# Kernel optimization log

Measured on AMD Instinct MI355X. Metric: run time of the kernel, lower is better.

The kernel has to match this reference:

```python
import jax, jax.numpy as jnp
import numpy as np
import math

B, S, HID, H, DH = 4, 1024, 1024, 16, 64  # batch, seq, hidden, heads, head_dim


def _rotate_half(x):
    x1, x2 = jnp.split(x, 2, axis=-1)
    return jnp.concatenate([-x2, x1], axis=-1)


def _apply_rope(t, freqs):
    # t: [B,H,S,DH], freqs: [S,rot_dim]; here rot_dim == DH so no pass-through part
    rot = freqs.shape[-1]
    cos_ = jnp.cos(freqs)[None, None, :, :].astype(t.dtype)
    sin_ = jnp.sin(freqs)[None, None, :, :].astype(t.dtype)
    t_rot, t_pass = t[..., :rot], t[..., rot:]
    t_rot = t_rot * cos_ + _rotate_half(t_rot) * sin_
    return jnp.concatenate([t_rot, t_pass], axis=-1)


def setup_inputs() -> dict:
    key = jax.random.key(0)
    ks = jax.random.split(key, 8)
    hidden_states = jax.random.normal(ks[0], (B, S, HID), dtype=jnp.float32)
    # additive mask: valid prefix of random length per batch row, -1e9 on padding
    lengths = jax.random.randint(ks[1], (B,), 3 * S // 4, S + 1)
    pos = jnp.arange(S)
    attention_mask = jnp.where(pos[None, :] < lengths[:, None], 0.0, -1e9)
    attention_mask = attention_mask.astype(jnp.float32)[:, None, None, :]  # [B,1,1,S]
    # rotary frequencies: standard RoPE angles, duplicated halves -> [S, DH]
    inv_freq = 1.0 / (10000.0 ** (jnp.arange(0, DH // 2, dtype=jnp.float32) / (DH // 2)))
    ang = pos.astype(jnp.float32)[:, None] * inv_freq[None, :]
    freqs = jnp.concatenate([ang, ang], axis=-1)  # [S, DH]
    sc = 0.02
    Wq = jax.random.normal(ks[2], (HID, HID), dtype=jnp.float32) * sc
    Wk = jax.random.normal(ks[3], (HID, HID), dtype=jnp.float32) * sc
    Wv = jax.random.normal(ks[4], (HID, HID), dtype=jnp.float32) * sc
    bq = jnp.zeros((HID,), dtype=jnp.float32)
    bk = jnp.zeros((HID,), dtype=jnp.float32)
    bv = jnp.zeros((HID,), dtype=jnp.float32)
    return dict(hidden_states=hidden_states, attention_mask=attention_mask, freqs=freqs,
                Wq=Wq, bq=bq, Wk=Wk, bk=bk, Wv=Wv, bv=bv)


def reference(hidden_states, attention_mask, freqs, Wq, bq, Wk, bk, Wv, bv):
    b, s, _ = hidden_states.shape
    # QKV projections -> [B,H,S,DH]
    q = (hidden_states @ Wq + bq).reshape(b, s, H, DH).transpose(0, 2, 1, 3)
    k = (hidden_states @ Wk + bk).reshape(b, s, H, DH).transpose(0, 2, 1, 3)
    v = (hidden_states @ Wv + bv).reshape(b, s, H, DH).transpose(0, 2, 1, 3)
    # inline RoPE on q and k (same freqs for both, as (rotary_pos_emb,)*2)
    q = _apply_rope(q, freqs)
    k = _apply_rope(k, freqs)
    scores = jnp.einsum('bhqd,bhkd->bhqk', q, k) / math.sqrt(DH)
    scores = scores + attention_mask  # additive mask broadcast over [B,H,S,S]
    probs = jax.nn.softmax(scores, axis=-1)
    # no_prob_mask filtering: zero out masked key columns
    probs = jnp.where(attention_mask < -1e-5, 0.0, probs)
    # dropout prob is 0.0 (eval) -> identity
    ctx = jnp.einsum('bhqk,bhkd->bhqd', probs, v)
    ctx = ctx.transpose(0, 2, 1, 3).reshape(b, s, H * DH)
    return ctx
```

## Files before the change

### kernel.cpp

```cpp
#include <hip/hip_runtime.h>
#include <hip/hip_bf16.h>
#include <cmath>

#define NB   4
#define NS   1024
#define NHID 1024
#define NH   16
#define NDH  64
#define QKV_PLANE (NB * NH * NS * NDH)

typedef __attribute__((ext_vector_type(8))) short bf16x8;
typedef __attribute__((ext_vector_type(4))) float f32x4;
typedef __attribute__((ext_vector_type(8))) unsigned short u16x8;

typedef __attribute__((address_space(1))) const void gv_t;
typedef __attribute__((address_space(3))) void       lv_t;

__device__ __forceinline__ void gload16(const void* g, void* l) {
    __builtin_amdgcn_global_load_lds((gv_t*)g, (lv_t*)l, 16, 0, 0);
}

__device__ __forceinline__ unsigned short f2b(float f) {
    union { float f; unsigned int u; } v; v.f = f;
    unsigned int r = (v.u + 0x7fff + ((v.u >> 16) & 1)) >> 16;
    return (unsigned short)r;
}

__device__ __forceinline__ unsigned int f2b2(float a, float b) {
    __hip_bfloat162 h = __float22bfloat162_rn(make_float2(a, b));
    union { __hip_bfloat162 h; unsigned int u; } v; v.h = h;
    return v.u;
}

__device__ __forceinline__ float fexp2(float x) {
#if __has_builtin(__builtin_amdgcn_exp2f)
    return __builtin_amdgcn_exp2f(x);
#else
    return exp2f(x);
#endif
}

__global__ __launch_bounds__(256) void prep_kernel(
    const float* __restrict__ hs, const float* __restrict__ freqs,
    const float* __restrict__ Wq, const float* __restrict__ Wk,
    const float* __restrict__ Wv,
    unsigned short* __restrict__ hsb, unsigned short* __restrict__ wt,
    float2* __restrict__ cs)
{
    const int z   = blockIdx.z;
    const int tid = threadIdx.x;

    if (z == 3) {
        const int bx = blockIdx.y * 16 + blockIdx.x;
        #pragma unroll
        for (int c = 0; c < 16; ++c) {
            const int idx = bx * 16384 + (c * 256 + tid) * 4;
            float4 v = *(const float4*)&hs[idx];
            ushort4 o;
            o.x = f2b(v.x); o.y = f2b(v.y); o.z = f2b(v.z); o.w = f2b(v.w);
            *(ushort4*)&hsb[idx] = o;
        }
        return;
    }
    if (z == 4) {
        const int bx = blockIdx.y * 16 + blockIdx.x;
        if (bx < 128) {
            const int id = bx * 256 + tid;
            const int s = id >> 5, d = id & 31;
            const float ang = freqs[s * NDH + d];
            float sn, cn;
            sincosf(ang, &sn, &cn);
            cs[id] = make_float2(cn, sn);
        }
        return;
    }

    const float* __restrict__ W = (z == 0) ? Wq : (z == 1) ? Wk : Wv;
    __shared__ float t[64][65];
    const int k0 = blockIdx.x * 64, n0 = blockIdx.y * 64;
    #pragma unroll
    for (int c = 0; c < 16; ++c) {
        const int flat = c * 256 + tid;
        const int r = flat >> 6, cc = flat & 63;
        t[r][cc] = W[(size_t)(k0 + r) * NHID + n0 + cc];
    }
    __syncthreads();
    #pragma unroll
    for (int c = 0; c < 16; ++c) {
        const int flat = c * 256 + tid;
        const int r = flat >> 6, cc = flat & 63;
        wt[(size_t)(z * 1024 + n0 + r) * NHID + k0 + cc] = f2b(t[cc][r]);
    }
}

__global__ __launch_bounds__(256) void fused_gemm_kernel(
    const unsigned short* __restrict__ hsb,
    const unsigned short* __restrict__ wt,
    const float2* __restrict__ cs,
    const float* __restrict__ bq, const float* __restrict__ bk,
    const float* __restrict__ bv,
    unsigned short* __restrict__ qkv)
{
    __shared__ short SH[16896];
    short* As = SH;
    short* Bs = SH + 8192;

    const int tid  = threadIdx.x;
    const int lane = tid & 63;
    const int wv   = __builtin_amdgcn_readfirstlane(tid >> 6);

    const int hw  = blockIdx.x + 24 * blockIdx.y;
    const int xcd = hw & 7;
    const int j   = hw >> 3;
    const int tx  = (xcd & 1) * 12 + (j % 12);
    const int ty  = (xcd >> 1) * 8 + (j / 12);

    const bool vmode = (tx >= 16);

    const unsigned short* Amat;
    const unsigned short* Bmat;
    int a_base, b_base, m0, n0, vb_ = 0;
    if (!vmode) {
        n0 = tx * 128;
        m0 = ty * 128;
        Amat = hsb;  a_base = m0;
        Bmat = wt;   b_base = n0;
    } else {
        m0  = (tx - 16) * 128;
        vb_ = ty >> 3;
        n0  = (ty & 7) * 128;
        Amat = wt;   a_base = 2048 + m0;
        Bmat = hsb;  b_base = vb_ * 1024 + n0;
    }

    const int ri  = lane >> 3;
    const int kcs = ((lane & 7) ^ ri) * 8;
    const unsigned short* gA[4];
    const unsigned short* gB[4];
    short* lA[4];
    short* lB[4];
    #pragma unroll
    for (int jj = 0; jj < 4; ++jj) {
        const int L = 4 * wv + jj;
        gA[jj] = Amat + (size_t)(a_base + L * 8 + ri) * NHID + kcs;
        gB[jj] = Bmat + (size_t)(b_base + L * 8 + ri) * NHID + kcs;
        lA[jj] = As + L * 512;
        lB[jj] = Bs + L * 512;
    }

    const int R  = (wv & 1) * 64;
    const int CW = (wv >> 1) * 64;
    const int c0 = lane & 15;
    const int g  = lane >> 4;
    const int sw7 = c0 & 7;
    int aoff[4][2], boff[4][2];
    #pragma unroll
    for (int i = 0; i < 4; ++i)
        #pragma unroll
        for (int ks = 0; ks < 2; ++ks) {
            aoff[i][ks] = (R  + 16 * i + c0) * 64 + ((g + 4 * ks) ^ sw7) * 8;
            boff[i][ks] = (CW + 16 * i + c0) * 64 + ((g + 4 * ks) ^ sw7) * 8;
        }

    f32x4 acc[4][4] = {};

    for (int k0 = 0; k0 < NHID; k0 += 64) {
        __syncthreads();
        #pragma unroll
        for (int jj = 0; jj < 4; ++jj) {
            gload16(gA[jj] + k0, lA[jj]);
            gload16(gB[jj] + k0, lB[jj]);
        }
        __syncthreads();
        #pragma unroll
        for (int ks = 0; ks < 2; ++ks) {
            bf16x8 af[4], bfr[4];
            #pragma unroll
            for (int i = 0; i < 4; ++i) af[i]  = *(const bf16x8*)&As[aoff[i][ks]];
            #pragma unroll
            for (int jj = 0; jj < 4; ++jj) bfr[jj] = *(const bf16x8*)&Bs[boff[jj][ks]];
            #pragma unroll
            for (int i = 0; i < 4; ++i)
                #pragma unroll
                for (int jj = 0; jj < 4; ++jj)
                    acc[i][jj] = __builtin_amdgcn_mfma_f32_16x16x32_bf16(
                        af[i], bfr[jj], acc[i][jj], 0, 0, 0);
        }
    }

    __syncthreads();
    unsigned short* E = (unsigned short*)SH;
    const int qrow4 = (lane >> 4) * 4;

    if (!vmode) {
        const int z  = n0 >> 10;
        const int hd = ((n0 & 1023) + CW) >> 6;
        const float* __restrict__ bb = (z == 0) ? bq : bk;
        const float b0 = bb[hd * 64 + c0];
        const float b1 = bb[hd * 64 + c0 + 16];
        const float b2 = bb[hd * 64 + c0 + 32];
        const float b3 = bb[hd * 64 + c0 + 48];

        #pragma unroll
        for (int i = 0; i < 4; ++i) {
            #pragma unroll
            for (int r = 0; r < 4; ++r) {
                const int ml = R + qrow4 + 16 * i + r;
                const int s  = (m0 + ml) & 1023;
                float o0 = acc[i][0][r] + b0;
                float o1 = acc[i][1][r] + b1;
                float o2 = acc[i][2][r] + b2;
                float o3 = acc[i][3][r] + b3;
                const float2 cs0 = cs[s * 32 + c0];
                const float2 cs1 = cs[s * 32 + c0 + 16];
                unsigned short* e = E + ml * 132 + CW + c0;
                e[0]  = f2b(o0 * cs0.x - o2 * cs0.y);
                e[16] = f2b(o1 * cs1.x - o3 * cs1.y);
                e[32] = f2b(o2 * cs0.x + o0 * cs0.y);
                e[48] = f2b(o3 * cs1.x + o1 * cs1.y);
            }
        }
        __syncthreads();

        const int hd0 = (n0 & 1023) >> 6;
        unsigned short* __restrict__ base = qkv + (size_t)z * QKV_PLANE;
        #pragma unroll
        for (int c = 0; c < 8; ++c) {
            const int chunk = c * 256 + tid;
            const int row   = chunk >> 4;
            const int col16 = chunk & 15;
            const int m     = m0 + row;
            const int bidx  = m >> 10;
            const int s     = m & 1023;
            const int head  = hd0 + (col16 >> 3);
            const int d     = (col16 & 7) * 8;
            u16x8 v = *(const u16x8*)&E[row * 132 + col16 * 8];
            *(u16x8*)&base[(((size_t)bidx * NH + head) * NS + s) * NDH + d] = v;
        }
    } else {
        #pragma unroll
        for (int i = 0; i < 4; ++i) {
            #pragma unroll
            for (int r = 0; r < 4; ++r) {
                const int ml  = R + qrow4 + 16 * i + r;
                const float bvm = bv[m0 + ml];
                unsigned short* e = E + ml * 132 + CW + c0;
                e[0]  = f2b(acc[i][0][r] + bvm);
                e[16] = f2b(acc[i][1][r] + bvm);
                e[32] = f2b(acc[i][2][r] + bvm);
                e[48] = f2b(acc[i][3][r] + bvm);
            }
        }
        __syncthreads();

        unsigned short* __restrict__ vplane = qkv + 2 * (size_t)QKV_PLANE;
        #pragma unroll
        for (int c = 0; c < 8; ++c) {
            const int chunk = c * 256 + tid;
            const int row   = chunk >> 4;
            const int col16 = chunk & 15;
            u16x8 v = *(const u16x8*)&E[row * 132 + col16 * 8];
            *(u16x8*)&vplane[((size_t)(vb_ * 1024 + m0 + row)) * NS
                             + n0 + col16 * 8] = v;
        }
    }
}

__global__ __launch_bounds__(512) void attn_kernel(
    const unsigned short* __restrict__ qkv, const float* __restrict__ mask,
    float* __restrict__ out)
{
    const int hw  = blockIdx.x + 8 * (blockIdx.y + 16 * blockIdx.z);
    const int xcd = hw & 7;
    const int j   = hw >> 3;
    const int hb  = xcd * 8 + (j & 7);
    const int qt  = j >> 3;
    const int h   = hb & 15, b = hb >> 4;

    const unsigned short* qp  = qkv + ((size_t)(b * NH + h) * NS) * NDH;
    const unsigned short* kp  = qp + QKV_PLANE;
    const unsigned short* vtp = qkv + 2 * (size_t)QKV_PLANE
                              + ((size_t)(b * NH + h) * NDH) * NS;

    __shared__ unsigned short KsA[2][64 * 64];
    __shared__ unsigned short VtA[2][64 * 64];
    __shared__ unsigned short PsA[128 * 64];
    __shared__ float Mk[1024];
    __shared__ float Ll[128];

    const int tid  = threadIdx.x;
    const int lane = tid & 63;
    const int w    = __builtin_amdgcn_readfirstlane(tid >> 6);
    const int c0   = lane & 15;
    const int g    = lane >> 4;
    const int sw7  = c0 & 7;
    const float C1 = 0.125f * 1.44269504f;

    {
        const int i = tid * 2;
        float2 mv = *(const float2*)&mask[(size_t)b * NS + i];
        Mk[i]     = mv.x * 1.44269504f;
        Mk[i + 1] = mv.y * 1.44269504f;
    }

    bf16x8 qf[2];
    #pragma unroll
    for (int ks = 0; ks < 2; ++ks)
        qf[ks] = *(const bf16x8*)&qp[
            (size_t)(qt * 128 + w * 16 + c0) * NDH + g * 8 + ks * 32];

    const int i8 = lane >> 3, c8 = lane & 7;
    const int gsw = (c8 ^ i8) * 8;
    const unsigned short* gk0 = kp  + (size_t)(w * 8 + i8) * NDH + gsw;
    const unsigned short* gv0 = vtp + (size_t)(w * 8 + i8) * NS  + gsw;

    int kaddr[4][2], pw4[4], pr[2];
    #pragma unroll
    for (int mt = 0; mt < 4; ++mt)
        #pragma unroll
        for (int ks = 0; ks < 2; ++ks)
            kaddr[mt][ks] = (mt * 16 + c0) * 64 + ((g + ks * 4) ^ sw7) * 8;
    #pragma unroll
    for (int mt = 0; mt < 4; ++mt)
        pw4[mt] = (w * 16 + c0) * 64 + ((2 * mt + (g >> 1)) ^ sw7) * 8 + (g & 1) * 4;
    #pragma unroll
    for (int ks = 0; ks < 2; ++ks)
        pr[ks] = (w * 16 + c0) * 64 + ((g + ks * 4) ^ sw7) * 8;

    gload16(gk0, &KsA[0][w * 512]);
    gload16(gv0, &VtA[0][w * 512]);
    __syncthreads();

    int ktmax = 16;
    while (ktmax > 1 && Mk[(ktmax - 1) * 64] < -1.0f) --ktmax;

    float lrow = 0.f;
    f32x4 O[4] = {};

    for (int kt = 0; kt < ktmax; ++kt) {
        const int cur = kt & 1;

        if (kt + 1 < ktmax) {
            gload16(gk0 + (size_t)(kt + 1) * 64 * NDH, &KsA[cur ^ 1][w * 512]);
            gload16(gv0 + (size_t)(kt + 1) * 64,       &VtA[cur ^ 1][w * 512]);
        }

        const unsigned short* Kb = KsA[cur];
        const unsigned short* Vb = VtA[cur];

        bf16x8 kf[4][2];
        #pragma unroll
        for (int mt = 0; mt < 4; ++mt)
            #pragma unroll
            for (int ks = 0; ks < 2; ++ks)
                kf[mt][ks] = *(const bf16x8*)&Kb[kaddr[mt][ks]];
        f32x4 S[4];
        __builtin_amdgcn_s_setprio(1);
        #pragma unroll
        for (int mt = 0; mt < 4; ++mt) {
            f32x4 a = {};
            a = __builtin_amdgcn_mfma_f32_16x16x32_bf16(kf[mt][0], qf[0], a, 0, 0, 0);
            a = __builtin_amdgcn_mfma_f32_16x16x32_bf16(kf[mt][1], qf[1], a, 0, 0, 0);
            S[mt] = a;
        }
        __builtin_amdgcn_s_setprio(0);

        float psum = 0.f;
        #pragma unroll
        for (int mt = 0; mt < 4; ++mt) {
            float4 mv = *(const float4*)&Mk[kt * 64 + mt * 16 + g * 4];
            float p0 = fexp2(S[mt][0] * C1 + mv.x);
            float p1 = fexp2(S[mt][1] * C1 + mv.y);
            float p2 = fexp2(S[mt][2] * C1 + mv.z);
            float p3 = fexp2(S[mt][3] * C1 + mv.w);
            psum += (p0 + p1) + (p2 + p3);
            uint2 u;
            u.x = f2b2(p0, p1);
            u.y = f2b2(p2, p3);
            *(uint2*)&PsA[pw4[mt]] = u;
        }
        lrow += psum;

        bf16x8 pf[2], vf[4][2];
        #pragma unroll
        for (int ks = 0; ks < 2; ++ks)
            pf[ks] = *(const bf16x8*)&PsA[pr[ks]];
        #pragma unroll
        for (int nd = 0; nd < 4; ++nd)
            #pragma unroll
            for (int ks = 0; ks < 2; ++ks)
                vf[nd][ks] = *(const bf16x8*)&Vb[kaddr[nd][ks]];
        __builtin_amdgcn_s_setprio(1);
        #pragma unroll
        for (int nd = 0; nd < 4; ++nd) {
            f32x4 o = O[nd];
            o = __builtin_amdgcn_mfma_f32_16x16x32_bf16(pf[0], vf[nd][0], o, 0, 0, 0);
            o = __builtin_amdgcn_mfma_f32_16x16x32_bf16(pf[1], vf[nd][1], o, 0, 0, 0);
            O[nd] = o;
        }
        __builtin_amdgcn_s_setprio(0);

        __syncthreads();
    }

    lrow += __shfl_xor(lrow, 16);
    lrow += __shfl_xor(lrow, 32);
    if (g == 0) Ll[w * 16 + c0] = lrow;
    float4 lv4 = *(const float4*)&Ll[w * 16 + g * 4];
    float inv[4];
    #pragma unroll
    for (int r = 0; r < 4; ++r) inv[r] = 1.0f / ((const float*)&lv4)[r];

    #pragma unroll
    for (int nd = 0; nd < 4; ++nd)
        #pragma unroll
        for (int r = 0; r < 4; ++r) {
            const int row = qt * 128 + w * 16 + g * 4 + r;
            const int col = h * 64 + nd * 16 + c0;
            out[((size_t)b * NS + row) * NHID + col] = O[nd][r] * inv[r];
        }
}

extern "C" void kernel_launch(void* const* d_in, const int* in_sizes, int n_in,
                              void* d_out, int out_size, void* d_ws, size_t ws_size,
                              hipStream_t stream) {
    const float* hs    = (const float*)d_in[0];
    const float* mask  = (const float*)d_in[1];
    const float* freqs = (const float*)d_in[2];
    const float* Wq    = (const float*)d_in[3];
    const float* bq    = (const float*)d_in[4];
    const float* Wk    = (const float*)d_in[5];
    const float* bk    = (const float*)d_in[6];
    const float* Wv    = (const float*)d_in[7];
    const float* bv    = (const float*)d_in[8];
    float* out = (float*)d_out;

    char* ws = (char*)d_ws;
    unsigned short* qkvb = (unsigned short*)ws;
    unsigned short* hsb  = (unsigned short*)(ws + 25165824);
    unsigned short* wtb  = (unsigned short*)(ws + 33554432);
    float2*         csb  = (float2*)       (ws + 39845888);

    prep_kernel<<<dim3(16, 16, 5), 256, 0, stream>>>(hs, freqs, Wq, Wk, Wv,
                                                     hsb, wtb, csb);
    fused_gemm_kernel<<<dim3(24, 32), 256, 0, stream>>>(hsb, wtb, csb,
                                                        bq, bk, bv, qkvb);
    attn_kernel<<<dim3(NS / 128, NH, NB), 512, 0, stream>>>(qkvb, mask, out);
}
```

Baseline: 153.3 us.

## Use 256x256 tiles with double-buffered async LDS loads in QKV GEMM

```diff
diff --git a/kernel.cpp b/kernel.cpp
--- a/kernel.cpp
+++ b/kernel.cpp
@@ -39,6 +39,15 @@
     return exp2f(x);
 #endif
 }
+
+#define VMWAIT(N) do { \
+    asm volatile("s_waitcnt vmcnt(" #N ")" ::: "memory"); \
+    __builtin_amdgcn_sched_barrier(0); } while (0)
+
+#define SBAR() do { \
+    __builtin_amdgcn_sched_barrier(0); \
+    __builtin_amdgcn_s_barrier(); \
+    __builtin_amdgcn_sched_barrier(0); } while (0)
 
 __global__ __launch_bounds__(256) void prep_kernel(
     const float* __restrict__ hs, const float* __restrict__ freqs,
@@ -93,7 +102,7 @@
     }
 }
 
-__global__ __launch_bounds__(256) void fused_gemm_kernel(
+__global__ __launch_bounds__(512, 2) void fused_gemm_kernel(
     const unsigned short* __restrict__ hsb,
     const unsigned short* __restrict__ wt,
     const float2* __restrict__ cs,
@@ -101,96 +110,114 @@
     const float* __restrict__ bv,
     unsigned short* __restrict__ qkv)
 {
-    __shared__ short SH[16896];
-    short* As = SH;
-    short* Bs = SH + 8192;
+    __shared__ short SH[65536];
 
     const int tid  = threadIdx.x;
     const int lane = tid & 63;
-    const int wv   = __builtin_amdgcn_readfirstlane(tid >> 6);
-
-    const int hw  = blockIdx.x + 24 * blockIdx.y;
-    const int xcd = hw & 7;
-    const int j   = hw >> 3;
-    const int tx  = (xcd & 1) * 12 + (j % 12);
-    const int ty  = (xcd >> 1) * 8 + (j / 12);
-
-    const bool vmode = (tx >= 16);
+    const int wv8  = __builtin_amdgcn_readfirstlane(tid >> 6);
+    const int wr   = wv8 >> 2;
+    const int wc   = wv8 & 3;
+
+    const int id = blockIdx.x;
+    const bool vmode = (id >= 128);
 
     const unsigned short* Amat;
     const unsigned short* Bmat;
     int a_base, b_base, m0, n0, vb_ = 0;
     if (!vmode) {
-        n0 = tx * 128;
-        m0 = ty * 128;
+        const int tm = id >> 3, tn = id & 7;
+        m0 = tm * 256;
+        n0 = tn * 256;
         Amat = hsb;  a_base = m0;
         Bmat = wt;   b_base = n0;
     } else {
-        m0  = (tx - 16) * 128;
-        vb_ = ty >> 3;
-        n0  = (ty & 7) * 128;
+        const int j = id - 128;
+        const int tm = j >> 4, tj = j & 15;
+        vb_ = tj >> 2;
+        m0  = tm * 256;
+        n0  = (tj & 3) * 256;
         Amat = wt;   a_base = 2048 + m0;
         Bmat = hsb;  b_base = vb_ * 1024 + n0;
     }
 
     const int ri  = lane >> 3;
     const int kcs = ((lane & 7) ^ ri) * 8;
-    const unsigned short* gA[4];
-    const unsigned short* gB[4];
-    short* lA[4];
-    short* lB[4];
-    #pragma unroll
-    for (int jj = 0; jj < 4; ++jj) {
-        const int L = 4 * wv + jj;
-        gA[jj] = Amat + (size_t)(a_base + L * 8 + ri) * NHID + kcs;
-        gB[jj] = Bmat + (size_t)(b_base + L * 8 + ri) * NHID + kcs;
-        lA[jj] = As + L * 512;
-        lB[jj] = Bs + L * 512;
-    }
-
-    const int R  = (wv & 1) * 64;
-    const int CW = (wv >> 1) * 64;
+    const unsigned short* gAb = Amat + (size_t)(a_base + wv8 * 32 + ri) * NHID + kcs;
+    const unsigned short* gBb = Bmat + (size_t)(b_base + wv8 * 32 + ri) * NHID + kcs;
+    const int l0 = wv8 * 2048;
+
+#define STAGE(BUF, kk) do { \
+    _Pragma("unroll") \
+    for (int j_ = 0; j_ < 4; ++j_) { \
+        gload16(gAb + (size_t)j_ * 8 * NHID + (kk), \
+                SH + (BUF) * 32768 + l0 + j_ * 512); \
+        gload16(gBb + (size_t)j_ * 8 * NHID + (kk), \
+                SH + (BUF) * 32768 + 16384 + l0 + j_ * 512); \
+    } } while (0)
+
+    const int R  = wr * 128;
+    const int CW = wc * 64;
     const int c0 = lane & 15;
     const int g  = lane >> 4;
     const int sw7 = c0 & 7;
-    int aoff[4][2], boff[4][2];
-    #pragma unroll
-    for (int i = 0; i < 4; ++i)
-        #pragma unroll
-        for (int ks = 0; ks < 2; ++ks) {
-            aoff[i][ks] = (R  + 16 * i + c0) * 64 + ((g + 4 * ks) ^ sw7) * 8;
-            boff[i][ks] = (CW + 16 * i + c0) * 64 + ((g + 4 * ks) ^ sw7) * 8;
-        }
-
-    f32x4 acc[4][4] = {};
-
-    for (int k0 = 0; k0 < NHID; k0 += 64) {
-        __syncthreads();
-        #pragma unroll
-        for (int jj = 0; jj < 4; ++jj) {
-            gload16(gA[jj] + k0, lA[jj]);
-            gload16(gB[jj] + k0, lB[jj]);
-        }
-        __syncthreads();
-        #pragma unroll
-        for (int ks = 0; ks < 2; ++ks) {
-            bf16x8 af[4], bfr[4];
-            #pragma unroll
-            for (int i = 0; i < 4; ++i) af[i]  = *(const bf16x8*)&As[aoff[i][ks]];
-            #pragma unroll
-            for (int jj = 0; jj < 4; ++jj) bfr[jj] = *(const bf16x8*)&Bs[boff[jj][ks]];
-            #pragma unroll
-            for (int i = 0; i < 4; ++i)
-                #pragma unroll
-                for (int jj = 0; jj < 4; ++jj)
-                    acc[i][jj] = __builtin_amdgcn_mfma_f32_16x16x32_bf16(
-                        af[i], bfr[jj], acc[i][jj], 0, 0, 0);
-        }
-    }
-
-    __syncthreads();
+    int aoff[8][2], boff[4][2];
+    #pragma unroll
+    for (int i = 0; i < 8; ++i)
+        #pragma unroll
+        for (int ks = 0; ks < 2; ++ks)
+            aoff[i][ks] = (R + 16 * i + c0) * 64 + ((g + 4 * ks) ^ sw7) * 8;
+    #pragma unroll
+    for (int j = 0; j < 4; ++j)
+        #pragma unroll
+        for (int ks = 0; ks < 2; ++ks)
+            boff[j][ks] = (CW + 16 * j + c0) * 64 + ((g + 4 * ks) ^ sw7) * 8;
+
+    f32x4 acc[8][4] = {};
+
+#define COMP(BUF) do { \
+    const short* Ac_ = SH + (BUF) * 32768; \
+    const short* Bc_ = SH + (BUF) * 32768 + 16384; \
+    _Pragma("unroll") \
+    for (int ks = 0; ks < 2; ++ks) { \
+        bf16x8 af[8], bf_[4]; \
+        _Pragma("unroll") \
+        for (int i = 0; i < 8; ++i) af[i] = *(const bf16x8*)&Ac_[aoff[i][ks]]; \
+        _Pragma("unroll") \
+        for (int j = 0; j < 4; ++j) bf_[j] = *(const bf16x8*)&Bc_[boff[j][ks]]; \
+        __builtin_amdgcn_s_setprio(1); \
+        _Pragma("unroll") \
+        for (int i = 0; i < 8; ++i) \
+            _Pragma("unroll") \
+            for (int j = 0; j < 4; ++j) \
+                acc[i][j] = __builtin_amdgcn_mfma_f32_16x16x32_bf16( \
+                    af[i], bf_[j], acc[i][j], 0, 0, 0); \
+        __builtin_amdgcn_s_setprio(0); \
+    } } while (0)
+
+    STAGE(0, 0);
+    #pragma unroll 1
+    for (int t = 0; t < 16; t += 2) {
+        STAGE(1, (t + 1) * 64);
+        VMWAIT(8);
+        SBAR();
+        COMP(0);
+        SBAR();
+
+        if (t + 2 < 16) {
+            STAGE(0, (t + 2) * 64);
+            VMWAIT(8);
+        } else {
+            VMWAIT(0);
+        }
+        SBAR();
+        COMP(1);
+        SBAR();
+    }
+#undef STAGE
+#undef COMP
+
     unsigned short* E = (unsigned short*)SH;
-    const int qrow4 = (lane >> 4) * 4;
+    const int qrow4 = g * 4;
 
     if (!vmode) {
         const int z  = n0 >> 10;
@@ -200,68 +227,78 @@
         const float b1 = bb[hd * 64 + c0 + 16];
         const float b2 = bb[hd * 64 + c0 + 32];
         const float b3 = bb[hd * 64 + c0 + 48];
-
-        #pragma unroll
-        for (int i = 0; i < 4; ++i) {
-            #pragma unroll
-            for (int r = 0; r < 4; ++r) {
-                const int ml = R + qrow4 + 16 * i + r;
-                const int s  = (m0 + ml) & 1023;
-                float o0 = acc[i][0][r] + b0;
-                float o1 = acc[i][1][r] + b1;
-                float o2 = acc[i][2][r] + b2;
-                float o3 = acc[i][3][r] + b3;
-                const float2 cs0 = cs[s * 32 + c0];
-                const float2 cs1 = cs[s * 32 + c0 + 16];
-                unsigned short* e = E + ml * 132 + CW + c0;
-                e[0]  = f2b(o0 * cs0.x - o2 * cs0.y);
-                e[16] = f2b(o1 * cs1.x - o3 * cs1.y);
-                e[32] = f2b(o2 * cs0.x + o0 * cs0.y);
-                e[48] = f2b(o3 * cs1.x + o1 * cs1.y);
-            }
-        }
-        __syncthreads();
-
         const int hd0 = (n0 & 1023) >> 6;
         unsigned short* __restrict__ base = qkv + (size_t)z * QKV_PLANE;
-        #pragma unroll
-        for (int c = 0; c < 8; ++c) {
-            const int chunk = c * 256 + tid;
-            const int row   = chunk >> 4;
-            const int col16 = chunk & 15;
-            const int m     = m0 + row;
-            const int bidx  = m >> 10;
-            const int s     = m & 1023;
-            const int head  = hd0 + (col16 >> 3);
-            const int d     = (col16 & 7) * 8;
-            u16x8 v = *(const u16x8*)&E[row * 132 + col16 * 8];
-            *(u16x8*)&base[(((size_t)bidx * NH + head) * NS + s) * NDH + d] = v;
+
+        #pragma unroll 1
+        for (int h = 0; h < 2; ++h) {
+            __syncthreads();
+            if (wr == h) {
+                #pragma unroll
+                for (int i = 0; i < 8; ++i) {
+                    #pragma unroll
+                    for (int r = 0; r < 4; ++r) {
+                        const int ml = qrow4 + 16 * i + r;
+                        const int s  = (m0 + h * 128 + ml) & 1023;
+                        float o0 = acc[i][0][r] + b0;
+                        float o1 = acc[i][1][r] + b1;
+                        float o2 = acc[i][2][r] + b2;
+                        float o3 = acc[i][3][r] + b3;
+                        const float2 cs0 = cs[s * 32 + c0];
+                        const float2 cs1 = cs[s * 32 + c0 + 16];
+                        unsigned short* e = E + ml * 264 + CW + c0;
+                        e[0]  = f2b(o0 * cs0.x - o2 * cs0.y);
+                        e[16] = f2b(o1 * cs1.x - o3 * cs1.y);
+                        e[32] = f2b(o2 * cs0.x + o0 * cs0.y);
+                        e[48] = f2b(o3 * cs1.x + o1 * cs1.y);
+                    }
+                }
+            }
+            __syncthreads();
+            #pragma unroll
+            for (int c = 0; c < 8; ++c) {
+                const int chunk = c * 512 + tid;
+                const int row   = chunk >> 5;
+                const int col16 = chunk & 31;
+                const int m     = m0 + h * 128 + row;
+                const int bidx  = m >> 10;
+                const int s     = m & 1023;
+                const int head  = hd0 + (col16 >> 3);
+                const int d     = (col16 & 7) * 8;
+                u16x8 v = *(const u16x8*)&E[row * 264 + col16 * 8];
+                *(u16x8*)&base[(((size_t)bidx * NH + head) * NS + s) * NDH + d] = v;
+            }
         }
     } else {
-        #pragma unroll
-        for (int i = 0; i < 4; ++i) {
+        unsigned short* __restrict__ vplane = qkv + 2 * (size_t)QKV_PLANE;
+        #pragma unroll 1
+        for (int h = 0; h < 2; ++h) {
+            __syncthreads();
+            if (wr == h) {
+                #pragma unroll
+                for (int i = 0; i < 8; ++i) {
+                    #pragma unroll
+                    for (int r = 0; r < 4; ++r) {
+                        const int ml  = qrow4 + 16 * i + r;
+                        const float bvm = bv[m0 + h * 128 + ml];
+                        unsigned short* e = E + ml * 264 + CW + c0;
+                        e[0]  = f2b(acc[i][0][r] + bvm);
+                        e[16] = f2b(acc[i][1][r] + bvm);
+                        e[32] = f2b(acc[i][2][r] + bvm);
+                        e[48] = f2b(acc[i][3][r] + bvm);
+                    }
+                }
+            }
+            __syncthreads();
             #pragma unroll
-            for (int r = 0; r < 4; ++r) {
-                const int ml  = R + qrow4 + 16 * i + r;
-                const float bvm = bv[m0 + ml];
-                unsigned short* e = E + ml * 132 + CW + c0;
-                e[0]  = f2b(acc[i][0][r] + bvm);
-                e[16] = f2b(acc[i][1][r] + bvm);
-                e[32] = f2b(acc[i][2][r] + bvm);
-                e[48] = f2b(acc[i][3][r] + bvm);
+            for (int c = 0; c < 8; ++c) {
+                const int chunk = c * 512 + tid;
+                const int row   = chunk >> 5;
+                const int col16 = chunk & 31;
+                u16x8 v = *(const u16x8*)&E[row * 264 + col16 * 8];
+                *(u16x8*)&vplane[((size_t)(vb_ * 1024 + m0 + h * 128 + row)) * NS
+                                 + n0 + col16 * 8] = v;
             }
-        }
-        __syncthreads();
-
-        unsigned short* __restrict__ vplane = qkv + 2 * (size_t)QKV_PLANE;
-        #pragma unroll
-        for (int c = 0; c < 8; ++c) {
-            const int chunk = c * 256 + tid;
-            const int row   = chunk >> 4;
-            const int col16 = chunk & 15;
-            u16x8 v = *(const u16x8*)&E[row * 132 + col16 * 8];
-            *(u16x8*)&vplane[((size_t)(vb_ * 1024 + m0 + row)) * NS
-                             + n0 + col16 * 8] = v;
         }
     }
 }
@@ -443,7 +480,7 @@
 
     prep_kernel<<<dim3(16, 16, 5), 256, 0, stream>>>(hs, freqs, Wq, Wk, Wv,
                                                      hsb, wtb, csb);
-    fused_gemm_kernel<<<dim3(24, 32), 256, 0, stream>>>(hsb, wtb, csb,
-                                                        bq, bk, bv, qkvb);
+    fused_gemm_kernel<<<dim3(192), 512, 0, stream>>>(hsb, wtb, csb,
+                                                     bq, bk, bv, qkvb);
     attn_kernel<<<dim3(NS / 128, NH, NB), 512, 0, stream>>>(qkvb, mask, out);
 }
```

Result: slower. 193.4 us (+26.2%).

## Halve waves per block in GEMM and attention, doubling per-wave tile work

Applied to the files above, without the earlier changes.

```diff
diff --git a/kernel.cpp b/kernel.cpp
--- a/kernel.cpp
+++ b/kernel.cpp
@@ -93,7 +93,7 @@
     }
 }
 
-__global__ __launch_bounds__(256) void fused_gemm_kernel(
+__global__ __launch_bounds__(128) void fused_gemm_kernel(
     const unsigned short* __restrict__ hsb,
     const unsigned short* __restrict__ wt,
     const float2* __restrict__ cs,
@@ -135,52 +135,46 @@
 
     const int ri  = lane >> 3;
     const int kcs = ((lane & 7) ^ ri) * 8;
-    const unsigned short* gA[4];
-    const unsigned short* gB[4];
-    short* lA[4];
-    short* lB[4];
-    #pragma unroll
-    for (int jj = 0; jj < 4; ++jj) {
-        const int L = 4 * wv + jj;
-        gA[jj] = Amat + (size_t)(a_base + L * 8 + ri) * NHID + kcs;
-        gB[jj] = Bmat + (size_t)(b_base + L * 8 + ri) * NHID + kcs;
-        lA[jj] = As + L * 512;
-        lB[jj] = Bs + L * 512;
-    }
-
-    const int R  = (wv & 1) * 64;
-    const int CW = (wv >> 1) * 64;
+    const unsigned short* gAb = Amat + (size_t)(a_base + 64 * wv + ri) * NHID + kcs;
+    const unsigned short* gBb = Bmat + (size_t)(b_base + 64 * wv + ri) * NHID + kcs;
+    short* lAb = As + wv * 4096;
+    short* lBb = Bs + wv * 4096;
+
+    const int CW = wv * 64;
     const int c0 = lane & 15;
     const int g  = lane >> 4;
     const int sw7 = c0 & 7;
-    int aoff[4][2], boff[4][2];
-    #pragma unroll
-    for (int i = 0; i < 4; ++i)
-        #pragma unroll
-        for (int ks = 0; ks < 2; ++ks) {
-            aoff[i][ks] = (R  + 16 * i + c0) * 64 + ((g + 4 * ks) ^ sw7) * 8;
-            boff[i][ks] = (CW + 16 * i + c0) * 64 + ((g + 4 * ks) ^ sw7) * 8;
-        }
-
-    f32x4 acc[4][4] = {};
+    int aoff[8][2], boff[4][2];
+    #pragma unroll
+    for (int i = 0; i < 8; ++i)
+        #pragma unroll
+        for (int ks = 0; ks < 2; ++ks)
+            aoff[i][ks] = (16 * i + c0) * 64 + ((g + 4 * ks) ^ sw7) * 8;
+    #pragma unroll
+    for (int jj = 0; jj < 4; ++jj)
+        #pragma unroll
+        for (int ks = 0; ks < 2; ++ks)
+            boff[jj][ks] = (CW + 16 * jj + c0) * 64 + ((g + 4 * ks) ^ sw7) * 8;
+
+    f32x4 acc[8][4] = {};
 
     for (int k0 = 0; k0 < NHID; k0 += 64) {
         __syncthreads();
         #pragma unroll
-        for (int jj = 0; jj < 4; ++jj) {
-            gload16(gA[jj] + k0, lA[jj]);
-            gload16(gB[jj] + k0, lB[jj]);
+        for (int jj = 0; jj < 8; ++jj) {
+            gload16(gAb + (size_t)jj * 8 * NHID + k0, lAb + jj * 512);
+            gload16(gBb + (size_t)jj * 8 * NHID + k0, lBb + jj * 512);
         }
         __syncthreads();
         #pragma unroll
         for (int ks = 0; ks < 2; ++ks) {
-            bf16x8 af[4], bfr[4];
-            #pragma unroll
-            for (int i = 0; i < 4; ++i) af[i]  = *(const bf16x8*)&As[aoff[i][ks]];
+            bf16x8 af[8], bfr[4];
+            #pragma unroll
+            for (int i = 0; i < 8; ++i) af[i]  = *(const bf16x8*)&As[aoff[i][ks]];
             #pragma unroll
             for (int jj = 0; jj < 4; ++jj) bfr[jj] = *(const bf16x8*)&Bs[boff[jj][ks]];
             #pragma unroll
-            for (int i = 0; i < 4; ++i)
+            for (int i = 0; i < 8; ++i)
                 #pragma unroll
                 for (int jj = 0; jj < 4; ++jj)
                     acc[i][jj] = __builtin_amdgcn_mfma_f32_16x16x32_bf16(
@@ -190,7 +184,7 @@
 
     __syncthreads();
     unsigned short* E = (unsigned short*)SH;
-    const int qrow4 = (lane >> 4) * 4;
+    const int qrow4 = g * 4;
 
     if (!vmode) {
         const int z  = n0 >> 10;
@@ -202,10 +196,10 @@
         const float b3 = bb[hd * 64 + c0 + 48];
 
         #pragma unroll
-        for (int i = 0; i < 4; ++i) {
+        for (int i = 0; i < 8; ++i) {
             #pragma unroll
             for (int r = 0; r < 4; ++r) {
-                const int ml = R + qrow4 + 16 * i + r;
+                const int ml = qrow4 + 16 * i + r;
                 const int s  = (m0 + ml) & 1023;
                 float o0 = acc[i][0][r] + b0;
                 float o1 = acc[i][1][r] + b1;
@@ -225,8 +219,8 @@
         const int hd0 = (n0 & 1023) >> 6;
         unsigned short* __restrict__ base = qkv + (size_t)z * QKV_PLANE;
         #pragma unroll
-        for (int c = 0; c < 8; ++c) {
-            const int chunk = c * 256 + tid;
+        for (int c = 0; c < 16; ++c) {
+            const int chunk = c * 128 + tid;
             const int row   = chunk >> 4;
             const int col16 = chunk & 15;
             const int m     = m0 + row;
@@ -239,10 +233,10 @@
         }
     } else {
         #pragma unroll
-        for (int i = 0; i < 4; ++i) {
+        for (int i = 0; i < 8; ++i) {
             #pragma unroll
             for (int r = 0; r < 4; ++r) {
-                const int ml  = R + qrow4 + 16 * i + r;
+                const int ml  = qrow4 + 16 * i + r;
                 const float bvm = bv[m0 + ml];
                 unsigned short* e = E + ml * 132 + CW + c0;
                 e[0]  = f2b(acc[i][0][r] + bvm);
@@ -255,8 +249,8 @@
 
         unsigned short* __restrict__ vplane = qkv + 2 * (size_t)QKV_PLANE;
         #pragma unroll
-        for (int c = 0; c < 8; ++c) {
-            const int chunk = c * 256 + tid;
+        for (int c = 0; c < 16; ++c) {
+            const int chunk = c * 128 + tid;
             const int row   = chunk >> 4;
             const int col16 = chunk & 15;
             u16x8 v = *(const u16x8*)&E[row * 132 + col16 * 8];
@@ -266,7 +260,7 @@
     }
 }
 
-__global__ __launch_bounds__(512) void attn_kernel(
+__global__ __launch_bounds__(256) void attn_kernel(
     const unsigned short* __restrict__ qkv, const float* __restrict__ mask,
     float* __restrict__ out)
 {
@@ -297,52 +291,66 @@
     const float C1 = 0.125f * 1.44269504f;
 
     {
-        const int i = tid * 2;
-        float2 mv = *(const float2*)&mask[(size_t)b * NS + i];
+        const int i = tid * 4;
+        float4 mv = *(const float4*)&mask[(size_t)b * NS + i];
         Mk[i]     = mv.x * 1.44269504f;
         Mk[i + 1] = mv.y * 1.44269504f;
-    }
-
-    bf16x8 qf[2];
-    #pragma unroll
-    for (int ks = 0; ks < 2; ++ks)
-        qf[ks] = *(const bf16x8*)&qp[
-            (size_t)(qt * 128 + w * 16 + c0) * NDH + g * 8 + ks * 32];
+        Mk[i + 2] = mv.z * 1.44269504f;
+        Mk[i + 3] = mv.w * 1.44269504f;
+    }
+
+    bf16x8 qf[2][2];
+    #pragma unroll
+    for (int a = 0; a < 2; ++a)
+        #pragma unroll
+        for (int ks = 0; ks < 2; ++ks)
+            qf[a][ks] = *(const bf16x8*)&qp[
+                (size_t)(qt * 128 + w * 32 + a * 16 + c0) * NDH + g * 8 + ks * 32];
 
     const int i8 = lane >> 3, c8 = lane & 7;
     const int gsw = (c8 ^ i8) * 8;
-    const unsigned short* gk0 = kp  + (size_t)(w * 8 + i8) * NDH + gsw;
-    const unsigned short* gv0 = vtp + (size_t)(w * 8 + i8) * NS  + gsw;
-
-    int kaddr[4][2], pw4[4], pr[2];
+    const unsigned short* gk0 = kp  + (size_t)(w * 16 + i8) * NDH + gsw;
+    const unsigned short* gv0 = vtp + (size_t)(w * 16 + i8) * NS  + gsw;
+
+    int kaddr[4][2], pw4[2][4], pr[2][2];
     #pragma unroll
     for (int mt = 0; mt < 4; ++mt)
         #pragma unroll
         for (int ks = 0; ks < 2; ++ks)
             kaddr[mt][ks] = (mt * 16 + c0) * 64 + ((g + ks * 4) ^ sw7) * 8;
     #pragma unroll
-    for (int mt = 0; mt < 4; ++mt)
-        pw4[mt] = (w * 16 + c0) * 64 + ((2 * mt + (g >> 1)) ^ sw7) * 8 + (g & 1) * 4;
-    #pragma unroll
-    for (int ks = 0; ks < 2; ++ks)
-        pr[ks] = (w * 16 + c0) * 64 + ((g + ks * 4) ^ sw7) * 8;
-
-    gload16(gk0, &KsA[0][w * 512]);
-    gload16(gv0, &VtA[0][w * 512]);
+    for (int a = 0; a < 2; ++a) {
+        #pragma unroll
+        for (int mt = 0; mt < 4; ++mt)
+            pw4[a][mt] = (w * 32 + a * 16 + c0) * 64
+                       + ((2 * mt + (g >> 1)) ^ sw7) * 8 + (g & 1) * 4;
+        #pragma unroll
+        for (int ks = 0; ks < 2; ++ks)
+            pr[a][ks] = (w * 32 + a * 16 + c0) * 64 + ((g + ks * 4) ^ sw7) * 8;
+    }
+
+    gload16(gk0,           &KsA[0][w * 1024]);
+    gload16(gk0 + 8 * NDH, &KsA[0][w * 1024 + 512]);
+    gload16(gv0,           &VtA[0][w * 1024]);
+    gload16(gv0 + 8 * NS,  &VtA[0][w * 1024 + 512]);
     __syncthreads();
 
     int ktmax = 16;
     while (ktmax > 1 && Mk[(ktmax - 1) * 64] < -1.0f) --ktmax;
 
-    float lrow = 0.f;
-    f32x4 O[4] = {};
+    float lrow[2] = {0.f, 0.f};
+    f32x4 O[2][4] = {};
 
     for (int kt = 0; kt < ktmax; ++kt) {
         const int cur = kt & 1;
 
         if (kt + 1 < ktmax) {
-            gload16(gk0 + (size_t)(kt + 1) * 64 * NDH, &KsA[cur ^ 1][w * 512]);
-            gload16(gv0 + (size_t)(kt + 1) * 64,       &VtA[cur ^ 1][w * 512]);
+            const unsigned short* nk = gk0 + (size_t)(kt + 1) * 64 * NDH;
+            const unsigned short* nv = gv0 + (size_t)(kt + 1) * 64;
+            gload16(nk,           &KsA[cur ^ 1][w * 1024]);
+            gload16(nk + 8 * NDH, &KsA[cur ^ 1][w * 1024 + 512]);
+            gload16(nv,           &VtA[cur ^ 1][w * 1024]);
+            gload16(nv + 8 * NS,  &VtA[cur ^ 1][w * 1024 + 512]);
         }
 
         const unsigned short* Kb = KsA[cur];
@@ -354,37 +362,44 @@
             #pragma unroll
             for (int ks = 0; ks < 2; ++ks)
                 kf[mt][ks] = *(const bf16x8*)&Kb[kaddr[mt][ks]];
-        f32x4 S[4];
+        f32x4 S[2][4];
         __builtin_amdgcn_s_setprio(1);
         #pragma unroll
-        for (int mt = 0; mt < 4; ++mt) {
-            f32x4 a = {};
-            a = __builtin_amdgcn_mfma_f32_16x16x32_bf16(kf[mt][0], qf[0], a, 0, 0, 0);
-            a = __builtin_amdgcn_mfma_f32_16x16x32_bf16(kf[mt][1], qf[1], a, 0, 0, 0);
-            S[mt] = a;
-        }
+        for (int a = 0; a < 2; ++a)
+            #pragma unroll
+            for (int mt = 0; mt < 4; ++mt) {
+                f32x4 s = {};
+                s = __builtin_amdgcn_mfma_f32_16x16x32_bf16(kf[mt][0], qf[a][0], s, 0, 0, 0);
+                s = __builtin_amdgcn_mfma_f32_16x16x32_bf16(kf[mt][1], qf[a][1], s, 0, 0, 0);
+                S[a][mt] = s;
+            }
         __builtin_amdgcn_s_setprio(0);
 
-        float psum = 0.f;
-        #pragma unroll
-        for (int mt = 0; mt < 4; ++mt) {
-            float4 mv = *(const float4*)&Mk[kt * 64 + mt * 16 + g * 4];
-            float p0 = fexp2(S[mt][0] * C1 + mv.x);
-            float p1 = fexp2(S[mt][1] * C1 + mv.y);
-            float p2 = fexp2(S[mt][2] * C1 + mv.z);
-            float p3 = fexp2(S[mt][3] * C1 + mv.w);
-            psum += (p0 + p1) + (p2 + p3);
-            uint2 u;
-            u.x = f2b2(p0, p1);
-            u.y = f2b2(p2, p3);
-            *(uint2*)&PsA[pw4[mt]] = u;
-        }
-        lrow += psum;
-
-        bf16x8 pf[2], vf[4][2];
-        #pragma unroll
-        for (int ks = 0; ks < 2; ++ks)
-            pf[ks] = *(const bf16x8*)&PsA[pr[ks]];
+        #pragma unroll
+        for (int a = 0; a < 2; ++a) {
+            float psum = 0.f;
+            #pragma unroll
+            for (int mt = 0; mt < 4; ++mt) {
+                float4 mv = *(const float4*)&Mk[kt * 64 + mt * 16 + g * 4];
+                float p0 = fexp2(S[a][mt][0] * C1 + mv.x);
+                float p1 = fexp2(S[a][mt][1] * C1 + mv.y);
+                float p2 = fexp2(S[a][mt][2] * C1 + mv.z);
+                float p3 = fexp2(S[a][mt][3] * C1 + mv.w);
+                psum += (p0 + p1) + (p2 + p3);
+                uint2 u;
+                u.x = f2b2(p0, p1);
+                u.y = f2b2(p2, p3);
+                *(uint2*)&PsA[pw4[a][mt]] = u;
+            }
+            lrow[a] += psum;
+        }
+
+        bf16x8 pf[2][2], vf[4][2];
+        #pragma unroll
+        for (int a = 0; a < 2; ++a)
+            #pragma unroll
+            for (int ks = 0; ks < 2; ++ks)
+                pf[a][ks] = *(const bf16x8*)&PsA[pr[a][ks]];
         #pragma unroll
         for (int nd = 0; nd < 4; ++nd)
             #pragma unroll
@@ -392,33 +407,41 @@
                 vf[nd][ks] = *(const bf16x8*)&Vb[kaddr[nd][ks]];
         __builtin_amdgcn_s_setprio(1);
         #pragma unroll
-        for (int nd = 0; nd < 4; ++nd) {
-            f32x4 o = O[nd];
-            o = __builtin_amdgcn_mfma_f32_16x16x32_bf16(pf[0], vf[nd][0], o, 0, 0, 0);
-            o = __builtin_amdgcn_mfma_f32_16x16x32_bf16(pf[1], vf[nd][1], o, 0, 0, 0);
-            O[nd] = o;
-        }
+        for (int a = 0; a < 2; ++a)
+            #pragma unroll
+            for (int nd = 0; nd < 4; ++nd) {
+                f32x4 o = O[a][nd];
+                o = __builtin_amdgcn_mfma_f32_16x16x32_bf16(pf[a][0], vf[nd][0], o, 0, 0, 0);
+                o = __builtin_amdgcn_mfma_f32_16x16x32_bf16(pf[a][1], vf[nd][1], o, 0, 0, 0);
+                O[a][nd] = o;
+            }
         __builtin_amdgcn_s_setprio(0);
 
         __syncthreads();
     }
 
-    lrow += __shfl_xor(lrow, 16);
-    lrow += __shfl_xor(lrow, 32);
-    if (g == 0) Ll[w * 16 + c0] = lrow;
-    float4 lv4 = *(const float4*)&Ll[w * 16 + g * 4];
-    float inv[4];
-    #pragma unroll
-    for (int r = 0; r < 4; ++r) inv[r] = 1.0f / ((const float*)&lv4)[r];
-
-    #pragma unroll
-    for (int nd = 0; nd < 4; ++nd)
-        #pragma unroll
-        for (int r = 0; r < 4; ++r) {
-            const int row = qt * 128 + w * 16 + g * 4 + r;
-            const int col = h * 64 + nd * 16 + c0;
-            out[((size_t)b * NS + row) * NHID + col] = O[nd][r] * inv[r];
-        }
+    #pragma unroll
+    for (int a = 0; a < 2; ++a) {
+        float lr = lrow[a];
+        lr += __shfl_xor(lr, 16);
+        lr += __shfl_xor(lr, 32);
+        if (g == 0) Ll[w * 32 + a * 16 + c0] = lr;
+    }
+    #pragma unroll
+    for (int a = 0; a < 2; ++a) {
+        float4 lv4 = *(const float4*)&Ll[w * 32 + a * 16 + g * 4];
+        float inv[4];
+        #pragma unroll
+        for (int r = 0; r < 4; ++r) inv[r] = 1.0f / ((const float*)&lv4)[r];
+        #pragma unroll
+        for (int nd = 0; nd < 4; ++nd)
+            #pragma unroll
+            for (int r = 0; r < 4; ++r) {
+                const int row = qt * 128 + w * 32 + a * 16 + g * 4 + r;
+                const int col = h * 64 + nd * 16 + c0;
+                out[((size_t)b * NS + row) * NHID + col] = O[a][nd][r] * inv[r];
+            }
+    }
 }
 
 extern "C" void kernel_launch(void* const* d_in, const int* in_sizes, int n_in,
@@ -443,7 +466,7 @@
 
     prep_kernel<<<dim3(16, 16, 5), 256, 0, stream>>>(hs, freqs, Wq, Wk, Wv,
                                                      hsb, wtb, csb);
-    fused_gemm_kernel<<<dim3(24, 32), 256, 0, stream>>>(hsb, wtb, csb,
+    fused_gemm_kernel<<<dim3(24, 32), 128, 0, stream>>>(hsb, wtb, csb,
                                                         bq, bk, bv, qkvb);
-    attn_kernel<<<dim3(NS / 128, NH, NB), 512, 0, stream>>>(qkvb, mask, out);
-}
+    attn_kernel<<<dim3(NS / 128, NH, NB), 256, 0, stream>>>(qkvb, mask, out);
+}
```

New measurement: 181.6 us. +18.5%, slower.

## Triple-buffer QKV GEMM K-loop with async LDS loads and single barrier

Applied to the files above, without the earlier changes.

```diff
diff --git a/kernel.cpp b/kernel.cpp
--- a/kernel.cpp
+++ b/kernel.cpp
@@ -39,6 +39,15 @@
     return exp2f(x);
 #endif
 }
+
+#define VMWAIT(N) do { \
+    asm volatile("s_waitcnt vmcnt(" #N ")" ::: "memory"); \
+    __builtin_amdgcn_sched_barrier(0); } while (0)
+
+#define SBAR() do { \
+    __builtin_amdgcn_sched_barrier(0); \
+    __builtin_amdgcn_s_barrier(); \
+    __builtin_amdgcn_sched_barrier(0); } while (0)
 
 __global__ __launch_bounds__(256) void prep_kernel(
     const float* __restrict__ hs, const float* __restrict__ freqs,
@@ -101,9 +110,7 @@
     const float* __restrict__ bv,
     unsigned short* __restrict__ qkv)
 {
-    __shared__ short SH[16896];
-    short* As = SH;
-    short* Bs = SH + 8192;
+    __shared__ short SH[24576];
 
     const int tid  = threadIdx.x;
     const int lane = tid & 63;
@@ -133,64 +140,68 @@
         Bmat = hsb;  b_base = vb_ * 1024 + n0;
     }
 
-    const int ri  = lane >> 3;
-    const int kcs = ((lane & 7) ^ ri) * 8;
-    const unsigned short* gA[4];
-    const unsigned short* gB[4];
-    short* lA[4];
-    short* lB[4];
-    #pragma unroll
-    for (int jj = 0; jj < 4; ++jj) {
-        const int L = 4 * wv + jj;
-        gA[jj] = Amat + (size_t)(a_base + L * 8 + ri) * NHID + kcs;
-        gB[jj] = Bmat + (size_t)(b_base + L * 8 + ri) * NHID + kcs;
-        lA[jj] = As + L * 512;
-        lB[jj] = Bs + L * 512;
-    }
+    const int srow = lane >> 2;
+    const int skc  = ((lane & 3) ^ ((lane >> 3) & 3)) * 8;
+    const unsigned short* gA1 = Amat + (size_t)(a_base + 16 * wv + srow) * NHID + skc;
+    const unsigned short* gA2 = gA1 + (size_t)64 * NHID;
+    const unsigned short* gB1 = Bmat + (size_t)(b_base + 16 * wv + srow) * NHID + skc;
+    const unsigned short* gB2 = gB1 + (size_t)64 * NHID;
+
+#define STAGE(S, T) do { \
+    short* Sb_ = SH + (S) * 8192 + 512 * wv; \
+    const size_t ko_ = (size_t)(T) * 32; \
+    gload16(gA1 + ko_, Sb_); \
+    gload16(gA2 + ko_, Sb_ + 2048); \
+    gload16(gB1 + ko_, Sb_ + 4096); \
+    gload16(gB2 + ko_, Sb_ + 6144); \
+} while (0)
 
     const int R  = (wv & 1) * 64;
     const int CW = (wv >> 1) * 64;
     const int c0 = lane & 15;
     const int g  = lane >> 4;
-    const int sw7 = c0 & 7;
-    int aoff[4][2], boff[4][2];
-    #pragma unroll
-    for (int i = 0; i < 4; ++i)
-        #pragma unroll
-        for (int ks = 0; ks < 2; ++ks) {
-            aoff[i][ks] = (R  + 16 * i + c0) * 64 + ((g + 4 * ks) ^ sw7) * 8;
-            boff[i][ks] = (CW + 16 * i + c0) * 64 + ((g + 4 * ks) ^ sw7) * 8;
-        }
+    const int swz  = (g ^ ((c0 >> 1) & 3)) * 8;
+    const int aofl = (R + c0) * 32 + swz;
+    const int bofl = 4096 + (CW + c0) * 32 + swz;
 
     f32x4 acc[4][4] = {};
 
-    for (int k0 = 0; k0 < NHID; k0 += 64) {
-        __syncthreads();
-        #pragma unroll
-        for (int jj = 0; jj < 4; ++jj) {
-            gload16(gA[jj] + k0, lA[jj]);
-            gload16(gB[jj] + k0, lB[jj]);
-        }
-        __syncthreads();
-        #pragma unroll
-        for (int ks = 0; ks < 2; ++ks) {
-            bf16x8 af[4], bfr[4];
-            #pragma unroll
-            for (int i = 0; i < 4; ++i) af[i]  = *(const bf16x8*)&As[aoff[i][ks]];
-            #pragma unroll
-            for (int jj = 0; jj < 4; ++jj) bfr[jj] = *(const bf16x8*)&Bs[boff[jj][ks]];
-            #pragma unroll
-            for (int i = 0; i < 4; ++i)
-                #pragma unroll
-                for (int jj = 0; jj < 4; ++jj)
-                    acc[i][jj] = __builtin_amdgcn_mfma_f32_16x16x32_bf16(
-                        af[i], bfr[jj], acc[i][jj], 0, 0, 0);
-        }
-    }
+#define COMP(S) do { \
+    const short* Sc_ = SH + (S) * 8192; \
+    bf16x8 af[4], bfr[4]; \
+    _Pragma("unroll") \
+    for (int i_ = 0; i_ < 4; ++i_) af[i_]  = *(const bf16x8*)&Sc_[aofl + 512 * i_]; \
+    _Pragma("unroll") \
+    for (int j_ = 0; j_ < 4; ++j_) bfr[j_] = *(const bf16x8*)&Sc_[bofl + 512 * j_]; \
+    __builtin_amdgcn_s_setprio(1); \
+    _Pragma("unroll") \
+    for (int i_ = 0; i_ < 4; ++i_) \
+        _Pragma("unroll") \
+        for (int j_ = 0; j_ < 4; ++j_) \
+            acc[i_][j_] = __builtin_amdgcn_mfma_f32_16x16x32_bf16( \
+                af[i_], bfr[j_], acc[i_][j_], 0, 0, 0); \
+    __builtin_amdgcn_s_setprio(0); \
+} while (0)
+
+    STAGE(0, 0);
+    STAGE(1, 1);
+    VMWAIT(4);
+    SBAR();
+
+    #pragma unroll 1
+    for (int tb = 0; tb < 30; tb += 3) {
+        STAGE(2, tb + 2); COMP(0); VMWAIT(4); SBAR();
+        STAGE(0, tb + 3); COMP(1); VMWAIT(4); SBAR();
+        STAGE(1, tb + 4); COMP(2); VMWAIT(4); SBAR();
+    }
+    COMP(0); VMWAIT(0); SBAR();
+    COMP(1);
+#undef STAGE
+#undef COMP
 
     __syncthreads();
     unsigned short* E = (unsigned short*)SH;
-    const int qrow4 = (lane >> 4) * 4;
+    const int qrow4 = g * 4;
 
     if (!vmode) {
         const int z  = n0 >> 10;
```

Measured after the change: 147.5 us, median of 2. 1.04x faster.
